# Kernel optimization log

Measured on AMD Instinct MI355X. Metric: run time of the kernel, lower is better.

The kernel has to match this reference:

```python
import jax, jax.numpy as jnp
import numpy as np

N = 50000   # nodes
E = 600000  # edges
D = 128     # in_feats = n_hidden
B = 16384   # pair batch
L = 2       # n_layers
C = 2       # n_classes
EPS = 1e-5


def setup_inputs() -> dict:
    key = jax.random.key(0)
    ks = jax.random.split(key, 16)
    s = 0.05
    return {
        "h": jax.random.normal(ks[0], (N, D), jnp.float32),
        "edge_src": jax.random.randint(ks[1], (E,), 0, N),
        "edge_dst": jax.random.randint(ks[2], (E,), 0, N),
        "x1": jax.random.randint(ks[3], (B,), 0, N),
        "x2": jax.random.randint(ks[4], (B,), 0, N),
        "x1_tar": jax.random.randint(ks[5], (B,), 0, N),
        "x2_tar": jax.random.randint(ks[6], (B,), 0, N),
        # SAGEConv params (mean aggregator): rst = h@W_self + mean_neigh@W_neigh + b
        "W_self": jax.random.normal(ks[7], (L, D, D), jnp.float32) * s,
        "W_neigh": jax.random.normal(ks[8], (L, D, D), jnp.float32) * s,
        "b_conv": jnp.zeros((L, D), jnp.float32),
        # head: linear1(3D->D) -> BN -> relu -> linear2(D->C)
        "W1": jax.random.normal(ks[9], (3 * D, D), jnp.float32) * s,
        "b1": jnp.zeros((D,), jnp.float32),
        "gamma": jnp.ones((D,), jnp.float32),
        "beta": jnp.zeros((D,), jnp.float32),
        "W2": jax.random.normal(ks[10], (D, C), jnp.float32) * s,
        "b2": jnp.zeros((C,), jnp.float32),
    }


def _sage_layers(h, edge_src, edge_dst, W_self, W_neigh, b_conv):
    # in-degree for mean aggregation (clamped to 1 to avoid div by 0)
    deg = jax.ops.segment_sum(jnp.ones((E,), h.dtype), edge_dst, num_segments=N)
    deg = jnp.maximum(deg, 1.0)[:, None]
    for l in range(L):
        msg = h[edge_src]                                        # [E, D] gather
        agg = jax.ops.segment_sum(msg, edge_dst, num_segments=N) / deg  # [N, D]
        h = jax.nn.relu(h @ W_self[l] + agg @ W_neigh[l] + b_conv[l])
    return h


def _pair_feat(h, a, b):
    ha, hb = h[a], h[b]
    return jnp.concatenate([ha, hb, jnp.abs(ha - hb)], axis=1)  # [B, 3D]


def _batchnorm(x, gamma, beta):
    m = x.mean(axis=0)
    v = x.var(axis=0)  # biased variance, as torch BN in training mode normalization
    return (x - m) * jax.lax.rsqrt(v + EPS) * gamma + beta


def reference(h, edge_src, edge_dst, x1, x2, x1_tar, x2_tar,
              W_self, W_neigh, b_conv, W1, b1, gamma, beta, W2, b2):
    h = _sage_layers(h, edge_src, edge_dst, W_self, W_neigh, b_conv)
    h_src = _pair_feat(h, x1, x2) @ W1 + b1
    h_tar = _pair_feat(h, x1_tar, x2_tar) @ W1 + b1
    h_src = _batchnorm(h_src, gamma, beta)
    h_tar = _batchnorm(h_tar, gamma, beta)
    h_src_mmd = jax.nn.relu(h_src)
    h_tar_mmd = jax.nn.relu(h_tar)
    h_p = h_src_mmd @ W2 + b2
    return (h_p, h_src_mmd, h_tar_mmd)
```

## Files before the change

kernel.cpp:

```cpp
#include <hip/hip_runtime.h>

#define NN 50000
#define NE 600000
#define DF 128
#define NB 16384

typedef short bf16x8 __attribute__((ext_vector_type(8)));
typedef float f32x4 __attribute__((ext_vector_type(4)));

__device__ __forceinline__ float bf2f(unsigned short u){
  return __uint_as_float(((unsigned int)u) << 16);
}
__device__ __forceinline__ unsigned short f2bf(float x){
  unsigned int b = __float_as_uint(x);
  return (unsigned short)((b + 0x7FFFu + ((b >> 16) & 1u)) >> 16);
}

__global__ void GraphSAGE_8504035246140_kernel(){ }

__global__ __launch_bounds__(256) void k_prelude(
    const float* h_in, unsigned short* h_c,
    const float* Ws, const float* Wn, const float* W1,
    unsigned short* WsB, unsigned short* WnB, unsigned short* W1B,
    int* cnt, float* stats){
  int b = blockIdx.x, t = threadIdx.x;
  if (b < 3125){
    int i = b * 256 + t;
    const float4* s = (const float4*)h_in;
    float4 v0 = s[i * 2], v1 = s[i * 2 + 1];
    unsigned short d[8] = {f2bf(v0.x), f2bf(v0.y), f2bf(v0.z), f2bf(v0.w),
                           f2bf(v1.x), f2bf(v1.y), f2bf(v1.z), f2bf(v1.w)};
    *(bf16x8*)(h_c + i * 8) = *(bf16x8*)d;
  } else if (b < 3516){
    int i = (b - 3125) * 256 + t;
    if (i < 2 * NN) cnt[i] = 0;
  } else if (b < 3518){
    int i = (b - 3516) * 256 + t;
    if (i < 512) stats[i] = 0.f;
  } else {
    int idx = (b - 3518) * 256 + t;
    if (idx < 2 * DF * DF){
      int layer = idx >> 14;
      int e = idx & (DF * DF - 1);
      int k = e >> 7, n = e & 127;
      int dst = layer * DF * DF + (((k >> 3) * 128 + n) << 3) + (k & 7);
      WsB[dst] = f2bf(Ws[idx]);
      WnB[dst] = f2bf(Wn[idx]);
    }
    if (idx < 3 * DF * DF){
      int k = idx >> 7, n = idx & 127;
      W1B[(((k >> 3) * 128 + n) << 3) + (k & 7)] = f2bf(W1[idx]);
    }
  }
}

__global__ void k_hist(const int* dst, int* cnt){
  int e = blockIdx.x * 256 + threadIdx.x;
  if (e < NE) atomicAdd(&cnt[dst[e]], 1);
}
__global__ void k_scan1(const int* cnt, int* bsum){
  __shared__ int l[256];
  int t = threadIdx.x, i = blockIdx.x * 256 + t;
  l[t] = (i < NN) ? cnt[i] : 0;
  __syncthreads();
  for (int o = 128; o > 0; o >>= 1){
    if (t < o) l[t] += l[t + o];
    __syncthreads();
  }
  if (t == 0) bsum[blockIdx.x] = l[0];
}
__global__ void k_scan3(const int* cnt, const int* bsum, int* rp, float* dinv){
  __shared__ int bs[256];
  __shared__ int l[256];
  int t = threadIdx.x, i = blockIdx.x * 256 + t;
  bs[t] = (t < 196) ? bsum[t] : 0;
  int v = (i < NN) ? cnt[i] : 0;
  l[t] = v;
  __syncthreads();
  for (int o = 1; o < 256; o <<= 1){
    int xb = (t >= o) ? bs[t - o] : 0;
    int xl = (t >= o) ? l[t - o] : 0;
    __syncthreads();
    bs[t] += xb; l[t] += xl;
    __syncthreads();
  }
  int base = (blockIdx.x == 0) ? 0 : bs[blockIdx.x - 1];
  if (i < NN){
    rp[i] = base + l[t] - v;
    dinv[i] = 1.0f / fmaxf((float)v, 1.0f);
    if (i == NN - 1) rp[NN] = base + l[t];
  }
}
__global__ void k_scatter(const int* src, const int* dst,
                          const int* rp, int* fill, int* perm){
  int e = blockIdx.x * 256 + threadIdx.x;
  if (e < NE){
    int d = dst[e];
    int pos = atomicAdd(&fill[d], 1);
    perm[rp[d] + pos] = src[e];
  }
}

__global__ __launch_bounds__(256) void k_agg(
    const unsigned int* hb32, const int* rp, const int* perm,
    const float* dinv, unsigned int* agg32){
  int n = blockIdx.x * 4 + (threadIdx.x >> 6);
  if (n >= NN) return;
  int l = threadIdx.x & 63;
  int half = l >> 5, lh = l & 31;
  int s = rp[n], e = rp[n + 1];
  float a0 = 0.f, a1 = 0.f, a2 = 0.f, a3 = 0.f;
  int i = s;
  for (; i + 8 <= e; i += 8){
    int p0 = perm[i + 0 + half];
    int p1 = perm[i + 2 + half];
    int p2 = perm[i + 4 + half];
    int p3 = perm[i + 6 + half];
    uint2 x0 = *(const uint2*)(hb32 + (size_t)p0 * 64 + lh * 2);
    uint2 x1 = *(const uint2*)(hb32 + (size_t)p1 * 64 + lh * 2);
    uint2 x2 = *(const uint2*)(hb32 + (size_t)p2 * 64 + lh * 2);
    uint2 x3 = *(const uint2*)(hb32 + (size_t)p3 * 64 + lh * 2);
    a0 += __uint_as_float(x0.x << 16); a1 += __uint_as_float(x0.x & 0xffff0000u);
    a2 += __uint_as_float(x0.y << 16); a3 += __uint_as_float(x0.y & 0xffff0000u);
    a0 += __uint_as_float(x1.x << 16); a1 += __uint_as_float(x1.x & 0xffff0000u);
    a2 += __uint_as_float(x1.y << 16); a3 += __uint_as_float(x1.y & 0xffff0000u);
    a0 += __uint_as_float(x2.x << 16); a1 += __uint_as_float(x2.x & 0xffff0000u);
    a2 += __uint_as_float(x2.y << 16); a3 += __uint_as_float(x2.y & 0xffff0000u);
    a0 += __uint_as_float(x3.x << 16); a1 += __uint_as_float(x3.x & 0xffff0000u);
    a2 += __uint_as_float(x3.y << 16); a3 += __uint_as_float(x3.y & 0xffff0000u);
  }
  if (i < e){
    int i0 = i + 0 + half, i1 = i + 2 + half, i2 = i + 4 + half, i3 = i + 6 + half;
    int p0 = perm[i0 < e ? i0 : s];
    int p1 = perm[i1 < e ? i1 : s];
    int p2 = perm[i2 < e ? i2 : s];
    int p3 = perm[i3 < e ? i3 : s];
    uint2 x0 = *(const uint2*)(hb32 + (size_t)p0 * 64 + lh * 2);
    uint2 x1 = *(const uint2*)(hb32 + (size_t)p1 * 64 + lh * 2);
    uint2 x2 = *(const uint2*)(hb32 + (size_t)p2 * 64 + lh * 2);
    uint2 x3 = *(const uint2*)(hb32 + (size_t)p3 * 64 + lh * 2);
    if (i0 < e){
      a0 += __uint_as_float(x0.x << 16); a1 += __uint_as_float(x0.x & 0xffff0000u);
      a2 += __uint_as_float(x0.y << 16); a3 += __uint_as_float(x0.y & 0xffff0000u);
    }
    if (i1 < e){
      a0 += __uint_as_float(x1.x << 16); a1 += __uint_as_float(x1.x & 0xffff0000u);
      a2 += __uint_as_float(x1.y << 16); a3 += __uint_as_float(x1.y & 0xffff0000u);
    }
    if (i2 < e){
      a0 += __uint_as_float(x2.x << 16); a1 += __uint_as_float(x2.x & 0xffff0000u);
      a2 += __uint_as_float(x2.y << 16); a3 += __uint_as_float(x2.y & 0xffff0000u);
    }
    if (i3 < e){
      a0 += __uint_as_float(x3.x << 16); a1 += __uint_as_float(x3.x & 0xffff0000u);
      a2 += __uint_as_float(x3.y << 16); a3 += __uint_as_float(x3.y & 0xffff0000u);
    }
  }
  a0 += __shfl_xor(a0, 32);
  a1 += __shfl_xor(a1, 32);
  a2 += __shfl_xor(a2, 32);
  a3 += __shfl_xor(a3, 32);
  if (half == 0){
    float di = dinv[n];
    uint2 r;
    r.x = (unsigned int)f2bf(a0 * di) | ((unsigned int)f2bf(a1 * di) << 16);
    r.y = (unsigned int)f2bf(a2 * di) | ((unsigned int)f2bf(a3 * di) << 16);
    *(uint2*)(agg32 + (size_t)n * 64 + lh * 2) = r;
  }
}

__global__ __launch_bounds__(256) void k_layer_mfma(
    const unsigned short* hb, const unsigned short* aggb,
    const unsigned short* WsB, const unsigned short* WnB,
    const float* bias, unsigned short* hout){
  int t = threadIdx.x;
  int w = t >> 6, l = t & 63;
  int m = l & 15, q = l >> 4;
  int r0 = blockIdx.x * 64 + w * 16;
  int arow = r0 + m; if (arow > NN - 1) arow = NN - 1;
  const unsigned short* hp = hb   + (size_t)arow * DF + q * 8;
  const unsigned short* ap = aggb + (size_t)arow * DF + q * 8;
  f32x4 acc[8];
  for (int ct = 0; ct < 8; ++ct){
    float bbc = bias[ct * 16 + m];
    acc[ct] = (f32x4){bbc, bbc, bbc, bbc};
  }
  for (int kt = 0; kt < 4; ++kt){
    bf16x8 a_h = *(const bf16x8*)(hp + kt * 32);
    bf16x8 a_g = *(const bf16x8*)(ap + kt * 32);
    int kg = kt * 4 + q;
    for (int ct = 0; ct < 8; ++ct){
      bf16x8 b_s = *(const bf16x8*)(WsB + (((kg << 7) + ct * 16 + m) << 3));
      bf16x8 b_n = *(const bf16x8*)(WnB + (((kg << 7) + ct * 16 + m) << 3));
      acc[ct] = __builtin_amdgcn_mfma_f32_16x16x32_bf16(a_h, b_s, acc[ct], 0, 0, 0);
      acc[ct] = __builtin_amdgcn_mfma_f32_16x16x32_bf16(a_g, b_n, acc[ct], 0, 0, 0);
    }
  }
  for (int ct = 0; ct < 8; ++ct){
    int col = ct * 16 + m;
    for (int reg = 0; reg < 4; ++reg){
      int row = r0 + q * 4 + reg;
      if (row < NN) hout[(size_t)row * DF + col] = f2bf(fmaxf(acc[ct][reg], 0.f));
    }
  }
}

__global__ __launch_bounds__(256) void k_pair_mfma(
    const unsigned short* h2,
    const int* x1, const int* x2, const int* x1t, const int* x2t,
    const unsigned short* W1B, const float* b1, float* zbase, float* stats){
  __shared__ __align__(16) unsigned short F[64 * 392];
  __shared__ float csum[128], csq[128];
  int g = blockIdx.y;
  const int* ia = g ? x1t : x1;
  const int* ib = g ? x2t : x2;
  float* z = zbase + (size_t)g * NB * DF;
  int t = threadIdx.x;
  if (t < 128){ csum[t] = 0.f; csq[t] = 0.f; }
  int r0 = blockIdx.x * 64;
  int i = t >> 2, qq = t & 3;
  int r = r0 + i;
  int a = ia[r], b = ib[r];
  const unsigned short* pa = h2 + (size_t)a * DF + qq * 32;
  const unsigned short* pb = h2 + (size_t)b * DF + qq * 32;
  unsigned short* fr = F + i * 392;
  for (int jj = 0; jj < 4; ++jj){
    bf16x8 va = *(const bf16x8*)(pa + jj * 8);
    bf16x8 vb = *(const bf16x8*)(pb + jj * 8);
    *(bf16x8*)(fr + qq * 32 + jj * 8) = va;
    *(bf16x8*)(fr + 128 + qq * 32 + jj * 8) = vb;
    unsigned short d[8];
    for (int e = 0; e < 8; ++e){
      float fa = bf2f((unsigned short)va[e]);
      float fb = bf2f((unsigned short)vb[e]);
      d[e] = f2bf(fabsf(fa - fb));
    }
    *(bf16x8*)(fr + 256 + qq * 32 + jj * 8) = *(bf16x8*)d;
  }
  __syncthreads();
  int w = t >> 6, l = t & 63;
  int m = l & 15, q = l >> 4;
  int rl = w * 16 + m;
  f32x4 acc[8];
  for (int ct = 0; ct < 8; ++ct){
    float bbc = b1[ct * 16 + m];
    acc[ct] = (f32x4){bbc, bbc, bbc, bbc};
  }
  for (int kt = 0; kt < 12; ++kt){
    bf16x8 af = *(const bf16x8*)(F + rl * 392 + kt * 32 + q * 8);
    int kg = kt * 4 + q;
    for (int ct = 0; ct < 8; ++ct){
      bf16x8 bfr = *(const bf16x8*)(W1B + (((kg << 7) + ct * 16 + m) << 3));
      acc[ct] = __builtin_amdgcn_mfma_f32_16x16x32_bf16(af, bfr, acc[ct], 0, 0, 0);
    }
  }
  for (int ct = 0; ct < 8; ++ct){
    int col = ct * 16 + m;
    int row = r0 + w * 16 + q * 4;
    float s = 0.f, s2 = 0.f;
    for (int reg = 0; reg < 4; ++reg){
      float v = acc[ct][reg];
      z[(size_t)(row + reg) * DF + col] = v;
      s += v; s2 += v * v;
    }
    atomicAdd(&csum[col], s);
    atomicAdd(&csq[col], s2);
  }
  __syncthreads();
  if (t < 128){
    atomicAdd(&stats[g * 256 + t], csum[t]);
    atomicAdd(&stats[g * 256 + 128 + t], csq[t]);
  }
}

__global__ __launch_bounds__(256) void k_norm_hp(
    const float* zbase, const float* stats,
    const float* gamma, const float* beta,
    const float* W2, const float* b2, float* mmd_base, float* hp){
  int g = blockIdx.y;
  int t = threadIdx.x;
  int w = t >> 6, l = t & 63;
  int c0 = l * 2, c1 = c0 + 1;
  float m0 = stats[g * 256 + c0] * (1.0f / NB);
  float m1 = stats[g * 256 + c1] * (1.0f / NB);
  float v0 = stats[g * 256 + 128 + c0] * (1.0f / NB) - m0 * m0;
  float v1 = stats[g * 256 + 128 + c1] * (1.0f / NB) - m1 * m1;
  float is0 = 1.0f / sqrtf(v0 + 1e-5f);
  float is1 = 1.0f / sqrtf(v1 + 1e-5f);
  float ga0 = gamma[c0], ga1 = gamma[c1];
  float be0 = beta[c0], be1 = beta[c1];
  float w200 = W2[c0 * 2], w201 = W2[c0 * 2 + 1];
  float w210 = W2[c1 * 2], w211 = W2[c1 * 2 + 1];
  const float* z = zbase + (size_t)g * NB * DF;
  float* mmd = mmd_base + (size_t)g * NB * DF;
  int rbase = blockIdx.x * 16 + w * 4;
  for (int rr = 0; rr < 4; ++rr){
    int row = rbase + rr;
    float2 zv = *(const float2*)(z + (size_t)row * DF + c0);
    float y0 = fmaxf((zv.x - m0) * is0 * ga0 + be0, 0.f);
    float y1 = fmaxf((zv.y - m1) * is1 * ga1 + be1, 0.f);
    float2 yv; yv.x = y0; yv.y = y1;
    *(float2*)(mmd + (size_t)row * DF + c0) = yv;
    if (g == 0){
      float s0 = y0 * w200 + y1 * w210;
      float s1 = y0 * w201 + y1 * w211;
      for (int o = 32; o > 0; o >>= 1){
        s0 += __shfl_xor(s0, o);
        s1 += __shfl_xor(s1, o);
      }
      if (l == 0){
        hp[row * 2]     = s0 + b2[0];
        hp[row * 2 + 1] = s1 + b2[1];
      }
    }
  }
}

extern "C" __attribute__((used, visibility("default")))
void kernel_launch(void* const* d_in, const int* in_sizes, int n_in,
                   void* d_out, int out_size, void* d_ws, size_t ws_size,
                   hipStream_t stream){
  const float* h_in  = (const float*)d_in[0];
  const int* esrc = (const int*)d_in[1];
  const int* edst = (const int*)d_in[2];
  const int* x1   = (const int*)d_in[3];
  const int* x2   = (const int*)d_in[4];
  const int* x1t  = (const int*)d_in[5];
  const int* x2t  = (const int*)d_in[6];
  const float* Wself = (const float*)d_in[7];
  const float* Wneigh= (const float*)d_in[8];
  const float* bconv = (const float*)d_in[9];
  const float* W1    = (const float*)d_in[10];
  const float* b1    = (const float*)d_in[11];
  const float* gamma = (const float*)d_in[12];
  const float* beta  = (const float*)d_in[13];
  const float* W2    = (const float*)d_in[14];
  const float* b2    = (const float*)d_in[15];
  float* out = (float*)d_out;
  float* hp_out   = out;
  float* mmd_base = out + 2 * NB;

  float* zreg  = (float*)d_ws;
  unsigned short* aggb = (unsigned short*)zreg;
  float* stats = zreg + (size_t)2 * NB * DF;
  float* mstd  = stats + 512;
  float* dinv  = mstd + 512;
  int* cnt  = (int*)(dinv + 50048);
  int* fill = cnt + NN;
  int* rp   = fill + NN;
  int* perm = rp + 50016;
  int* bsum = perm + 600000;
  unsigned short* h_c = (unsigned short*)(bsum + 256);
  unsigned short* h1b = h_c + (size_t)NN * DF;
  unsigned short* h2b = h_c;
  unsigned short* WsB = h1b + (size_t)NN * DF;
  unsigned short* WnB = WsB + 2 * DF * DF;
  unsigned short* W1B = WnB + 2 * DF * DF;

  k_prelude<<<3710, 256, 0, stream>>>(h_in, h_c, Wself, Wneigh, W1,
                                      WsB, WnB, W1B, cnt, stats);

  k_hist<<<(NE + 255) / 256, 256, 0, stream>>>(edst, cnt);
  k_scan1<<<196, 256, 0, stream>>>(cnt, bsum);
  k_scan3<<<196, 256, 0, stream>>>(cnt, bsum, rp, dinv);
  k_scatter<<<(NE + 255) / 256, 256, 0, stream>>>(esrc, edst, rp, fill, perm);

  k_agg<<<(NN + 3) / 4, 256, 0, stream>>>((const unsigned int*)h_c, rp, perm,
                                          dinv, (unsigned int*)aggb);
  k_layer_mfma<<<(NN + 63) / 64, 256, 0, stream>>>(h_c, aggb, WsB, WnB, bconv, h1b);
  k_agg<<<(NN + 3) / 4, 256, 0, stream>>>((const unsigned int*)h1b, rp, perm,
                                          dinv, (unsigned int*)aggb);
  k_layer_mfma<<<(NN + 63) / 64, 256, 0, stream>>>(h1b, aggb, WsB + DF * DF,
                                                   WnB + DF * DF, bconv + DF, h2b);

  k_pair_mfma<<<dim3(NB / 64, 2), 256, 0, stream>>>(h2b, x1, x2, x1t, x2t,
                                                    W1B, b1, zreg, stats);
  k_norm_hp<<<dim3(NB / 16, 2), 256, 0, stream>>>(zreg, stats, gamma, beta,
                                                  W2, b2, mmd_base, hp_out);
}
```

Baseline: 292.6 us.

## Split aggregation feature dimension across four blocks with eight edge slots per wave

The neighbor aggregation kernel now splits each node's 128-wide feature row into four quarter segments handled by separate blocks, so grid size grows fourfold. Each wave processes eight edges in parallel (8 lanes per edge, 64B per edge segment) instead of two, reducing the per-node serial loop length for average degree ~12. The cost is that each block re-reads the perm indices four times, gathers become 64-byte segments instead of 256-byte rows, and a three-stage shuffle reduction replaces one.

```diff
diff --git a/kernel.cpp b/kernel.cpp
--- a/kernel.cpp
+++ b/kernel.cpp
@@ -104,22 +104,24 @@
 __global__ __launch_bounds__(256) void k_agg(
     const unsigned int* hb32, const int* rp, const int* perm,
     const float* dinv, unsigned int* agg32){
-  int n = blockIdx.x * 4 + (threadIdx.x >> 6);
+  int qd = blockIdx.x & 3;
+  int n = (blockIdx.x >> 2) * 4 + (threadIdx.x >> 6);
   if (n >= NN) return;
   int l = threadIdx.x & 63;
-  int half = l >> 5, lh = l & 31;
+  int slot = l >> 3, li = l & 7;
   int s = rp[n], e = rp[n + 1];
+  const unsigned int* hq = hb32 + qd * 16 + li * 2;
   float a0 = 0.f, a1 = 0.f, a2 = 0.f, a3 = 0.f;
   int i = s;
-  for (; i + 8 <= e; i += 8){
-    int p0 = perm[i + 0 + half];
-    int p1 = perm[i + 2 + half];
-    int p2 = perm[i + 4 + half];
-    int p3 = perm[i + 6 + half];
-    uint2 x0 = *(const uint2*)(hb32 + (size_t)p0 * 64 + lh * 2);
-    uint2 x1 = *(const uint2*)(hb32 + (size_t)p1 * 64 + lh * 2);
-    uint2 x2 = *(const uint2*)(hb32 + (size_t)p2 * 64 + lh * 2);
-    uint2 x3 = *(const uint2*)(hb32 + (size_t)p3 * 64 + lh * 2);
+  for (; i + 32 <= e; i += 32){
+    int p0 = perm[i + slot];
+    int p1 = perm[i + 8 + slot];
+    int p2 = perm[i + 16 + slot];
+    int p3 = perm[i + 24 + slot];
+    uint2 x0 = *(const uint2*)(hq + (size_t)p0 * 64);
+    uint2 x1 = *(const uint2*)(hq + (size_t)p1 * 64);
+    uint2 x2 = *(const uint2*)(hq + (size_t)p2 * 64);
+    uint2 x3 = *(const uint2*)(hq + (size_t)p3 * 64);
     a0 += __uint_as_float(x0.x << 16); a1 += __uint_as_float(x0.x & 0xffff0000u);
     a2 += __uint_as_float(x0.y << 16); a3 += __uint_as_float(x0.y & 0xffff0000u);
     a0 += __uint_as_float(x1.x << 16); a1 += __uint_as_float(x1.x & 0xffff0000u);
@@ -130,15 +132,15 @@
     a2 += __uint_as_float(x3.y << 16); a3 += __uint_as_float(x3.y & 0xffff0000u);
   }
   if (i < e){
-    int i0 = i + 0 + half, i1 = i + 2 + half, i2 = i + 4 + half, i3 = i + 6 + half;
+    int i0 = i + slot, i1 = i + 8 + slot, i2 = i + 16 + slot, i3 = i + 24 + slot;
     int p0 = perm[i0 < e ? i0 : s];
     int p1 = perm[i1 < e ? i1 : s];
     int p2 = perm[i2 < e ? i2 : s];
     int p3 = perm[i3 < e ? i3 : s];
-    uint2 x0 = *(const uint2*)(hb32 + (size_t)p0 * 64 + lh * 2);
-    uint2 x1 = *(const uint2*)(hb32 + (size_t)p1 * 64 + lh * 2);
-    uint2 x2 = *(const uint2*)(hb32 + (size_t)p2 * 64 + lh * 2);
-    uint2 x3 = *(const uint2*)(hb32 + (size_t)p3 * 64 + lh * 2);
+    uint2 x0 = *(const uint2*)(hq + (size_t)p0 * 64);
+    uint2 x1 = *(const uint2*)(hq + (size_t)p1 * 64);
+    uint2 x2 = *(const uint2*)(hq + (size_t)p2 * 64);
+    uint2 x3 = *(const uint2*)(hq + (size_t)p3 * 64);
     if (i0 < e){
       a0 += __uint_as_float(x0.x << 16); a1 += __uint_as_float(x0.x & 0xffff0000u);
       a2 += __uint_as_float(x0.y << 16); a3 += __uint_as_float(x0.y & 0xffff0000u);
@@ -156,16 +158,18 @@
       a2 += __uint_as_float(x3.y << 16); a3 += __uint_as_float(x3.y & 0xffff0000u);
     }
   }
-  a0 += __shfl_xor(a0, 32);
-  a1 += __shfl_xor(a1, 32);
-  a2 += __shfl_xor(a2, 32);
-  a3 += __shfl_xor(a3, 32);
-  if (half == 0){
+  a0 += __shfl_xor(a0, 8);  a1 += __shfl_xor(a1, 8);
+  a2 += __shfl_xor(a2, 8);  a3 += __shfl_xor(a3, 8);
+  a0 += __shfl_xor(a0, 16); a1 += __shfl_xor(a1, 16);
+  a2 += __shfl_xor(a2, 16); a3 += __shfl_xor(a3, 16);
+  a0 += __shfl_xor(a0, 32); a1 += __shfl_xor(a1, 32);
+  a2 += __shfl_xor(a2, 32); a3 += __shfl_xor(a3, 32);
+  if (slot == 0){
     float di = dinv[n];
     uint2 r;
     r.x = (unsigned int)f2bf(a0 * di) | ((unsigned int)f2bf(a1 * di) << 16);
     r.y = (unsigned int)f2bf(a2 * di) | ((unsigned int)f2bf(a3 * di) << 16);
-    *(uint2*)(agg32 + (size_t)n * 64 + lh * 2) = r;
+    *(uint2*)(agg32 + (size_t)n * 64 + qd * 16 + li * 2) = r;
   }
 }
 
@@ -365,11 +369,11 @@
   k_scan3<<<196, 256, 0, stream>>>(cnt, bsum, rp, dinv);
   k_scatter<<<(NE + 255) / 256, 256, 0, stream>>>(esrc, edst, rp, fill, perm);
 
-  k_agg<<<(NN + 3) / 4, 256, 0, stream>>>((const unsigned int*)h_c, rp, perm,
-                                          dinv, (unsigned int*)aggb);
+  k_agg<<<12500 * 4, 256, 0, stream>>>((const unsigned int*)h_c, rp, perm,
+                                       dinv, (unsigned int*)aggb);
   k_layer_mfma<<<(NN + 63) / 64, 256, 0, stream>>>(h_c, aggb, WsB, WnB, bconv, h1b);
-  k_agg<<<(NN + 3) / 4, 256, 0, stream>>>((const unsigned int*)h1b, rp, perm,
-                                          dinv, (unsigned int*)aggb);
+  k_agg<<<12500 * 4, 256, 0, stream>>>((const unsigned int*)h1b, rp, perm,
+                                       dinv, (unsigned int*)aggb);
   k_layer_mfma<<<(NN + 63) / 64, 256, 0, stream>>>(h1b, aggb, WsB + DF * DF,
                                                    WnB + DF * DF, bconv + DF, h2b);
 
```

Result: slower. 374.8 us (+28.1%).
